# Kernel tuning notes

Hardware: AMD Instinct MI355X
Metric: run time of the kernel (lower is better)

The kernel has to match this reference:

```python
import jax, jax.numpy as jnp
import numpy as np

N, E, D, H, C, L = 10000, 160000, 512, 4, 128, 2  # nodes, edges, feat dim, heads, dim/head, layers


def setup_inputs() -> dict:
    key = jax.random.key(0)
    ks = jax.random.split(key, 16)
    s = 0.05  # weight scale (xavier-like)
    return {
        "x": jax.random.normal(ks[0], (N, D), jnp.float32),
        "edge_index": jax.random.randint(ks[1], (2, E), 0, N, dtype=jnp.int64),
        "edge_attr": jax.random.uniform(ks[2], (E, 1), jnp.float32),
        "Wq": jax.random.normal(ks[3], (L, D, H * C), jnp.float32) * s,
        "bq": jnp.zeros((L, H * C), jnp.float32),
        "Wk": jax.random.normal(ks[4], (L, D, H * C), jnp.float32) * s,
        "bk": jnp.zeros((L, H * C), jnp.float32),
        "Wv": jax.random.normal(ks[5], (L, D, H * C), jnp.float32) * s,
        "bv": jnp.zeros((L, H * C), jnp.float32),
        "We": jax.random.normal(ks[6], (L, 1, H * C), jnp.float32) * s,
        "Ws": jax.random.normal(ks[7], (L, D, H * C), jnp.float32) * s,
        "bs": jnp.zeros((L, H * C), jnp.float32),
        "gn_w": jnp.ones((L, H * C), jnp.float32),
        "gn_b": jnp.zeros((L, H * C), jnp.float32),
        "gn_ms": jnp.ones((L, H * C), jnp.float32),
    }


def _forward(x, edge_index, edge_attr, Wq, bq, Wk, bk, Wv, bv, We, Ws, bs, gn_w, gn_b, gn_ms):
    src, dst = edge_index[0], edge_index[1]
    h = x
    scale = 1.0 / jnp.sqrt(jnp.float32(C))
    for l in range(L):
        q = (h @ Wq[l] + bq[l]).reshape(N, H, C)
        k = (h @ Wk[l] + bk[l]).reshape(N, H, C)
        v = (h @ Wv[l] + bv[l]).reshape(N, H, C)
        e = (edge_attr @ We[l]).reshape(E, H, C)
        kj = k[src] + e                                    # [E,H,C]
        logits = jnp.einsum('ehc,ehc->eh', q[dst], kj) * scale  # [E,H]
        m = jax.ops.segment_max(logits, dst, num_segments=N)
        m = jnp.where(jnp.isfinite(m), m, 0.0)
        a = jnp.exp(logits - m[dst])
        denom = jax.ops.segment_sum(a, dst, num_segments=N)
        alpha = a / (denom[dst] + 1e-16)                   # scatter-softmax over in-edges
        msg = (v[src] + e) * alpha[:, :, None]             # [E,H,C]
        out = jax.ops.segment_sum(msg, dst, num_segments=N).reshape(N, H * C)
        out = out + h @ Ws[l] + bs[l]                      # root/skip connection
        # GraphNorm (single graph): mean over nodes
        mean = out.mean(0)
        sub = out - gn_ms[l] * mean
        var = (sub * sub).mean(0)
        out = gn_w[l] * sub * jax.lax.rsqrt(var + 1e-5) + gn_b[l]
        h = jax.nn.relu(out)
    xt = h.T @ h                                           # [D,D] gram matrix
    xt = (xt - xt.min()) / (xt.max() - xt.min() + 1e-8)
    iu = jnp.triu_indices(xt.shape[0], k=1)
    return xt[iu].reshape(-1, 1)


def reference(x, edge_index, edge_attr, Wq, bq, Wk, bk, Wv, bv, We, Ws, bs, gn_w, gn_b, gn_ms):
    return _forward(x, edge_index, edge_attr, Wq, bq, Wk, bk, Wv, bv, We, Ws, bs, gn_w, gn_b, gn_ms)
```

## Files before the change

### kernel.cpp

```cpp
#include <hip/hip_runtime.h>
#include <math.h>
#include <stdint.h>

typedef unsigned short u16;
typedef __attribute__((ext_vector_type(8))) _Float16 f16x8;
typedef __attribute__((ext_vector_type(4))) float f32x4;

constexpr int NN = 10000;
constexpr int NE = 160000;
constexpr int DD = 512;
constexpr int NL = 2;
constexpr int MPAD = 10112;
constexpr int K2 = 512;
constexpr int NC = 2048;
constexpr int GZ = 32;
constexpr int NKT = K2 / 32;
constexpr float SCALE = 0.08838834764831845f;

constexpr size_t B_C   = 0;
constexpr size_t B_XT  = (size_t)10016 * NC * 4;
constexpr size_t B_SM  = B_XT + (size_t)262144 * 4;
constexpr size_t B_A2  = B_SM + 32768;
constexpr size_t B_B2T = B_A2 + (size_t)MPAD * K2 * 2;
constexpr size_t B_INT = B_B2T + (size_t)2 * NC * K2 * 2;
constexpr size_t SM_CS = 0, SM_CQ = 512, SM_CA = 1024, SM_CB = 1536;
constexpr size_t SM_PMN = 2048, SM_PMX = 2304, SM_MM = 2560, SM_BIAS = 2688;
constexpr size_t I_INDPTR = 0;
constexpr size_t I_CNT    = 10016;
constexpr size_t I_CUR    = 20032;
constexpr size_t I_SSRC   = 30048;
constexpr size_t I_SATTR  = 190048;

__device__ __forceinline__ u16 f2h(float v) {
    _Float16 h = (_Float16)v;
    union { _Float16 h; u16 u; } x; x.h = h;
    return x.u;
}
__device__ __forceinline__ float h2f(u16 b) {
    union { u16 u; _Float16 h; } y; y.u = b;
    return (float)y.h;
}
__device__ __forceinline__ void gload16(const u16* g, u16* l) {
    __builtin_amdgcn_global_load_lds(
        (const __attribute__((address_space(1))) void*)g,
        (__attribute__((address_space(3))) void*)l, 16, 0, 0);
}
__device__ __forceinline__ void tile_pair(int p, int& ti, int& tj) {
    ti = (p < 4) ? 0 : (p < 7) ? 1 : (p < 9) ? 2 : 3;
    tj = p - ((ti == 0) ? 0 : (ti == 1) ? 3 : (ti == 2) ? 5 : 6);
}

__global__ void hist_kernel(const int* __restrict__ dst, int* __restrict__ cnt) {
    int e = blockIdx.x * 256 + threadIdx.x;
    if (e < NE) atomicAdd(&cnt[dst[e]], 1);
}

__global__ void scan_kernel(const int* __restrict__ cnt, int* __restrict__ indptr,
                            int* __restrict__ cur) {
    __shared__ int sh[1024];
    int tid = threadIdx.x;
    int carry = 0;
    for (int base = 0; base < NN; base += 1024) {
        int idx = base + tid;
        int v = (idx < NN) ? cnt[idx] : 0;
        sh[tid] = v;
        __syncthreads();
        #pragma unroll
        for (int off = 1; off < 1024; off <<= 1) {
            int t = (tid >= off) ? sh[tid - off] : 0;
            __syncthreads();
            sh[tid] += t;
            __syncthreads();
        }
        int incl = sh[tid];
        int excl = incl - v;
        if (idx < NN) { indptr[idx] = carry + excl; cur[idx] = carry + excl; }
        int total = sh[1023];
        __syncthreads();
        carry += total;
    }
    if (tid == 0) indptr[NN] = carry;
}

__global__ void scatter_kernel(const int* __restrict__ src, const int* __restrict__ dst,
                               const float* __restrict__ eattr, int* __restrict__ cur,
                               int* __restrict__ ssrc, float* __restrict__ sattr) {
    int e = blockIdx.x * 256 + threadIdx.x;
    if (e < NE) {
        int d = dst[e];
        int p = atomicAdd(&cur[d], 1);
        ssrc[p]  = src[e];
        sattr[p] = eattr[e];
    }
}

__global__ void convert_x_kernel(const float* __restrict__ x, u16* __restrict__ A2) {
    size_t idx = (size_t)blockIdx.x * 256 + threadIdx.x;
    if (idx >= (size_t)MPAD * 512) return;
    int r = (int)(idx >> 9), c = (int)(idx & 511);
    float v = (r < NN) ? x[(size_t)r * 512 + c] : 0.f;
    A2[(size_t)r * K2 + c] = f2h(v);
}

__global__ void convert_w_kernel(const float* __restrict__ Wq, const float* __restrict__ Wk,
                                 const float* __restrict__ Wv, const float* __restrict__ Ws,
                                 u16* __restrict__ B2T) {
    __shared__ float t[64][65];
    int bz = blockIdx.z; int l = bz >> 2, m = bz & 3;
    const float* W = (m == 0 ? Wq : m == 1 ? Wk : m == 2 ? Wv : Ws) + (size_t)l * 512 * 512;
    int k0 = blockIdx.x * 64, n0 = blockIdx.y * 64;
    int tx = threadIdx.x, ty = threadIdx.y;
    #pragma unroll
    for (int i = 0; i < 16; i++) {
        int kk = ty + 4 * i;
        t[kk][tx] = W[(size_t)(k0 + kk) * 512 + n0 + tx];
    }
    __syncthreads();
    u16* B = B2T + (size_t)l * NC * K2;
    #pragma unroll
    for (int i = 0; i < 16; i++) {
        int nn = ty + 4 * i;
        B[(size_t)(m * 512 + n0 + nn) * K2 + k0 + tx] = f2h(t[tx][nn]);
    }
}

__global__ void convert_b_kernel(const float* __restrict__ bq, const float* __restrict__ bk,
                                 const float* __restrict__ bv, const float* __restrict__ bs,
                                 float* __restrict__ biascat) {
    int idx = blockIdx.x * 256 + threadIdx.x;
    if (idx >= 2 * NC) return;
    int l = idx >> 11, c = idx & 2047;
    int m = c >> 9, j = c & 511;
    const float* b = (m == 0 ? bq : m == 1 ? bk : m == 2 ? bv : bs);
    biascat[idx] = b[l * 512 + j];
}

__global__ __launch_bounds__(256) void gemm_mfma(
    const u16* __restrict__ A2, const u16* __restrict__ B2T,
    const float* __restrict__ biasc, float* __restrict__ C)
{
    __shared__ u16 As[4096];
    __shared__ u16 Bs[4096];
    int tid = threadIdx.x;
    int wave = tid >> 6, lane = tid & 63;
    int wr = wave >> 1, wc = wave & 1;

    int bid = blockIdx.x;
    int xcd = bid & 7, qq = bid >> 3;
    int half = (qq >= 79) ? 1 : 0;
    int mb = qq - half * 79;
    int nb = xcd * 2 + half;
    int row0 = mb * 128, col0 = nb * 128;
    int mtype = nb >> 2;

    int ar0 = tid >> 2;
    int ac0 = (tid & 3) * 8;
    const u16* gA = A2  + (size_t)(row0 + ar0) * K2 + ac0;
    const u16* gB = B2T + (size_t)(col0 + ar0) * K2 + ac0;
    u16* lA = &As[wave * 512];
    u16* lB = &Bs[wave * 512];

    f32x4 acc[4][4];
    #pragma unroll
    for (int m = 0; m < 4; ++m)
        #pragma unroll
        for (int n = 0; n < 4; ++n) acc[m][n] = (f32x4){0.f, 0.f, 0.f, 0.f};

    int frow = lane & 15, fk = (lane >> 4) * 8;

    for (int kt = 0; kt < NKT; ++kt) {
        gload16(gA,             lA);
        gload16(gA + 64 * K2,   lA + 2048);
        gload16(gB,             lB);
        gload16(gB + 64 * K2,   lB + 2048);
        gA += 32; gB += 32;
        __syncthreads();
        f16x8 af[4], bfr[4];
        #pragma unroll
        for (int m = 0; m < 4; ++m)
            af[m] = *reinterpret_cast<const f16x8*>(&As[(wr * 64 + m * 16 + frow) * 32 + fk]);
        #pragma unroll
        for (int n = 0; n < 4; ++n)
            bfr[n] = *reinterpret_cast<const f16x8*>(&Bs[(wc * 64 + n * 16 + frow) * 32 + fk]);
        #pragma unroll
        for (int m = 0; m < 4; ++m)
            #pragma unroll
            for (int n = 0; n < 4; ++n)
                acc[m][n] = __builtin_amdgcn_mfma_f32_16x16x32_f16(af[m], bfr[n], acc[m][n], 0, 0, 0);
        __syncthreads();
    }

    u16* KV = (u16*)C;
    int rq = lane >> 4;
    #pragma unroll
    for (int n = 0; n < 4; ++n) {
        int gc = col0 + wc * 64 + n * 16 + frow;
        float bv = biasc[gc];
        #pragma unroll
        for (int m = 0; m < 4; ++m) {
            int gr0 = row0 + wr * 64 + m * 16 + rq * 4;
            #pragma unroll
            for (int r = 0; r < 4; ++r) {
                int gr = gr0 + r;
                if (gr < NN) {
                    float val = acc[m][n][r] + bv;
                    if (mtype == 0 || mtype == 3) C[(size_t)gr * NC + gc] = val;
                    else                          KV[(size_t)gr * 4096 + 512 + gc] = f2h(val);
                }
            }
        }
    }
}

__global__ __launch_bounds__(256) void agg_kernel(
    float* __restrict__ C, const float* __restrict__ Wel,
    const int* __restrict__ indptr, const int* __restrict__ ssrc,
    const float* __restrict__ sattr)
{
    int wid  = threadIdx.x >> 6;
    int lane = threadIdx.x & 63;
    int n = blockIdx.x * 4 + wid;
    if (n >= NN) return;
    int base = lane * 8;
    const u16* KV = (const u16*)C;

    const float4* qp = (const float4*)(C + (size_t)n * NC + base);
    float4 q0 = qp[0], q1 = qp[1];
    float qv[8] = {q0.x,q0.y,q0.z,q0.w,q1.x,q1.y,q1.z,q1.w};
    float we[8];
    #pragma unroll
    for (int j = 0; j < 8; j++) we[j] = Wel[base + j];

    float t = 0.f;
    #pragma unroll
    for (int j = 0; j < 8; j++) t = fmaf(qv[j], we[j], t);
    #pragma unroll
    for (int m = 1; m < 16; m <<= 1) t += __shfl_xor(t, m, 64);
    float qWe = t;

    float mrun = -1e30f, msum = 0.f, cattr = 0.f;
    float acc[8] = {0.f,0.f,0.f,0.f,0.f,0.f,0.f,0.f};
    int p0 = indptr[n], p1 = indptr[n + 1];
    for (int p = p0; p < p1; ++p) {
        int s = ssrc[p];
        float at = sattr[p];
        union { uint4 u; u16 h[8]; } kr, vr;
        kr.u = *(const uint4*)(KV + (size_t)s * 4096 + 1024 + base);
        float d = 0.f;
        #pragma unroll
        for (int j = 0; j < 8; j++) d = fmaf(qv[j], h2f(kr.h[j]), d);
        #pragma unroll
        for (int m = 1; m < 16; m <<= 1) d += __shfl_xor(d, m, 64);
        float logit = (d + at * qWe) * SCALE;
        float mnew = fmaxf(mrun, logit);
        float r = __expf(mrun - mnew);
        float a = __expf(logit - mnew);
        vr.u = *(const uint4*)(KV + (size_t)s * 4096 + 1536 + base);
        msum  = msum  * r + a;
        cattr = cattr * r + a * at;
        #pragma unroll
        for (int j = 0; j < 8; j++) acc[j] = acc[j] * r + a * h2f(vr.h[j]);
        mrun = mnew;
    }
    float inv = 1.f / (msum + 1e-16f);
    float* op = C + (size_t)n * NC + 1536 + base;
    float4 o0 = *(float4*)op, o1 = *(float4*)(op + 4);
    float ov[8] = {o0.x,o0.y,o0.z,o0.w,o1.x,o1.y,o1.z,o1.w};
    #pragma unroll
    for (int j = 0; j < 8; j++) ov[j] += (acc[j] + cattr * we[j]) * inv;
    *(float4*)op       = make_float4(ov[0], ov[1], ov[2], ov[3]);
    *(float4*)(op + 4) = make_float4(ov[4], ov[5], ov[6], ov[7]);
}

__global__ void colstat_kernel(const float* __restrict__ C,
                               float* __restrict__ cs, float* __restrict__ cq) {
    int c = threadIdx.x;
    int r0 = blockIdx.x * 125;
    float s0 = 0, s1 = 0, q0 = 0, q1 = 0;
    for (int r = r0; r < r0 + 125; ++r) {
        float v0 = C[(size_t)r * NC + 1536 + c];
        float v1 = C[(size_t)r * NC + 1536 + c + 256];
        s0 += v0; q0 += v0 * v0;
        s1 += v1; q1 += v1 * v1;
    }
    atomicAdd(&cs[c], s0);       atomicAdd(&cq[c], q0);
    atomicAdd(&cs[c + 256], s1); atomicAdd(&cq[c + 256], q1);
}

__global__ void coef_kernel(const float* __restrict__ cs, const float* __restrict__ cq,
                            const float* __restrict__ gnw, const float* __restrict__ gnb,
                            const float* __restrict__ gnm,
                            float* __restrict__ Aa, float* __restrict__ Bb) {
    int c = blockIdx.x * 256 + threadIdx.x;
    if (c >= DD) return;
    float mean = cs[c] * (1.f / NN);
    float ex2  = cq[c] * (1.f / NN);
    float ms = gnm[c];
    float var = ex2 - (2.f * ms - ms * ms) * mean * mean;
    float A = gnw[c] * rsqrtf(var + 1e-5f);
    Aa[c] = A;
    Bb[c] = gnb[c] - A * ms * mean;
}

__global__ void normrelu_kernel(const float* __restrict__ C, const float* __restrict__ Aa,
                                const float* __restrict__ Bb, u16* __restrict__ A2) {
    for (size_t idx = (size_t)blockIdx.x * 256 + threadIdx.x; idx < (size_t)NN * 512;
         idx += (size_t)2048 * 256) {
        int r = (int)(idx >> 9), c = (int)(idx & 511);
        float v = fmaxf(fmaf(Aa[c], C[(size_t)r * NC + 1536 + c], Bb[c]), 0.f);
        A2[(size_t)r * K2 + c] = f2h(v);
    }
}

__global__ __launch_bounds__(256) void gram_part_kernel(const u16* __restrict__ A2,
                                                        float* __restrict__ part) {
    __shared__ u16 LA[128][40], LB[128][40];
    int b = blockIdx.x;
    int p = b >> 5, z = b & (GZ - 1);
    int ti, tj; tile_pair(p, ti, tj);
    int i0c = ti * 128, j0c = tj * 128;
    int st0 = (z * 316) / GZ, st1 = ((z + 1) * 316) / GZ;

    int t = threadIdx.x;
    int c = t & 127, nb = t >> 7;
    int wave = t >> 6, lane = t & 63;
    int wr = wave >> 1, wc = wave & 1;
    int frow = lane & 15, fk = (lane >> 4) * 8, rq = lane >> 4;

    f32x4 acc[4][4];
    #pragma unroll
    for (int m = 0; m < 4; ++m)
        #pragma unroll
        for (int n = 0; n < 4; ++n) acc[m][n] = (f32x4){0.f, 0.f, 0.f, 0.f};

    for (int st = st0; st < st1; ++st) {
        int node0 = st * 32 + nb * 16;
        uint4 bufA4[2], bufB4[2];
        u16* ba = (u16*)bufA4; u16* bb = (u16*)bufB4;
        #pragma unroll
        for (int i = 0; i < 16; i++) {
            const u16* rp = A2 + (size_t)(node0 + i) * K2;
            ba[i] = rp[i0c + c];
            bb[i] = rp[j0c + c];
        }
        __syncthreads();
        *(uint4*)&LA[c][nb * 16]     = bufA4[0];
        *(uint4*)&LA[c][nb * 16 + 8] = bufA4[1];
        *(uint4*)&LB[c][nb * 16]     = bufB4[0];
        *(uint4*)&LB[c][nb * 16 + 8] = bufB4[1];
        __syncthreads();
        f16x8 af[4], bfr[4];
        #pragma unroll
        for (int m = 0; m < 4; ++m)
            af[m] = *reinterpret_cast<const f16x8*>(&LA[wr * 64 + m * 16 + frow][fk]);
        #pragma unroll
        for (int n = 0; n < 4; ++n)
            bfr[n] = *reinterpret_cast<const f16x8*>(&LB[wc * 64 + n * 16 + frow][fk]);
        #pragma unroll
        for (int m = 0; m < 4; ++m)
            #pragma unroll
            for (int n = 0; n < 4; ++n)
                acc[m][n] = __builtin_amdgcn_mfma_f32_16x16x32_f16(af[m], bfr[n], acc[m][n], 0, 0, 0);
    }

    float* pp = part + ((size_t)b << 14);
    #pragma unroll
    for (int m = 0; m < 4; ++m) {
        int li0 = wr * 64 + m * 16 + rq * 4;
        #pragma unroll
        for (int n = 0; n < 4; ++n) {
            int lj = wc * 64 + n * 16 + frow;
            #pragma unroll
            for (int r = 0; r < 4; ++r)
                pp[(li0 + r) * 128 + lj] = acc[m][n][r];
        }
    }
}

__global__ __launch_bounds__(256) void gram_reduce_kernel(const float* __restrict__ part,
                                                          float* __restrict__ xt,
                                                          float* __restrict__ pmn,
                                                          float* __restrict__ pmx) {
    __shared__ float smn[256], smx[256];
    int tid = threadIdx.x;
    int g = blockIdx.x * 1024 + tid * 4;
    int p = g >> 14, idx = g & 16383;
    const float* bp = part + ((size_t)p * GZ << 14) + idx;
    float4 s = make_float4(0.f, 0.f, 0.f, 0.f);
    #pragma unroll
    for (int z = 0; z < GZ; ++z) {
        float4 v = *(const float4*)(bp + (size_t)z * 16384);
        s.x += v.x; s.y += v.y; s.z += v.z; s.w += v.w;
    }
    int ti, tj; tile_pair(p, ti, tj);
    int li = idx >> 7, lj = idx & 127;
    *(float4*)&xt[(size_t)(ti * 128 + li) * DD + tj * 128 + lj] = s;
    float mn = fminf(fminf(s.x, s.y), fminf(s.z, s.w));
    float mx = fmaxf(fmaxf(s.x, s.y), fmaxf(s.z, s.w));
    smn[tid] = mn; smx[tid] = mx;
    __syncthreads();
    for (int st = 128; st > 0; st >>= 1) {
        if (tid < st) {
            smn[tid] = fminf(smn[tid], smn[tid + st]);
            smx[tid] = fmaxf(smx[tid], smx[tid + st]);
        }
        __syncthreads();
    }
    if (tid == 0) { pmn[blockIdx.x] = smn[0]; pmx[blockIdx.x] = smx[0]; }
}

__global__ void minmax2_kernel(const float* __restrict__ pmn, const float* __restrict__ pmx,
                               float* __restrict__ mm) {
    __shared__ float smn[256], smx[256];
    int tid = threadIdx.x;
    smn[tid] = (tid < 160) ? pmn[tid] : 1e30f;
    smx[tid] = (tid < 160) ? pmx[tid] : -1e30f;
    __syncthreads();
    for (int s = 128; s > 0; s >>= 1) {
        if (tid < s) { smn[tid] = fminf(smn[tid], smn[tid + s]); smx[tid] = fmaxf(smx[tid], smx[tid + s]); }
        __syncthreads();
    }
    if (tid == 0) { mm[0] = smn[0]; mm[1] = smx[0]; }
}

__global__ void final_kernel(const float* __restrict__ xt, const float* __restrict__ mm,
                             float* __restrict__ outp) {
    int idx = blockIdx.x * 256 + threadIdx.x;
    if (idx >= 262144) return;
    int i = idx >> 9, j = idx & 511;
    if (j <= i) return;
    float mn = mm[0], mx = mm[1];
    float v = (xt[idx] - mn) / (mx - mn + 1e-8f);
    int p = i * 511 - (i * (i - 1)) / 2 + (j - i - 1);
    outp[p] = v;
}

extern "C" void kernel_launch(void* const* d_in, const int* in_sizes, int n_in,
                              void* d_out, int out_size, void* d_ws, size_t ws_size,
                              hipStream_t stream) {
    const float* x     = (const float*)d_in[0];
    const int*   ei    = (const int*)d_in[1];
    const float* eattr = (const float*)d_in[2];
    const float* Wq = (const float*)d_in[3];  const float* bq = (const float*)d_in[4];
    const float* Wk = (const float*)d_in[5];  const float* bk = (const float*)d_in[6];
    const float* Wv = (const float*)d_in[7];  const float* bv = (const float*)d_in[8];
    const float* We = (const float*)d_in[9];
    const float* Ws = (const float*)d_in[10]; const float* bs = (const float*)d_in[11];
    const float* gnw = (const float*)d_in[12];
    const float* gnb = (const float*)d_in[13];
    const float* gnm = (const float*)d_in[14];

    char*  wsb = (char*)d_ws;
    float* C    = (float*)(wsb + B_C);
    float* xt   = (float*)(wsb + B_XT);
    float* sm   = (float*)(wsb + B_SM);
    u16*   A2   = (u16*)(wsb + B_A2);
    u16*   B2T  = (u16*)(wsb + B_B2T);
    int*   wsI  = (int*)(wsb + B_INT);

    const int* src = ei;
    const int* dst = ei + NE;

    convert_x_kernel<<<(MPAD * 512) / 256, 256, 0, stream>>>(x, A2);
    convert_w_kernel<<<dim3(8, 8, 8), dim3(64, 4), 0, stream>>>(Wq, Wk, Wv, Ws, B2T);
    convert_b_kernel<<<16, 256, 0, stream>>>(bq, bk, bv, bs, sm + SM_BIAS);

    hipMemsetAsync(wsI + I_CNT, 0, NN * sizeof(int), stream);
    hist_kernel<<<(NE + 255) / 256, 256, 0, stream>>>(dst, wsI + I_CNT);
    scan_kernel<<<1, 1024, 0, stream>>>(wsI + I_CNT, wsI + I_INDPTR, wsI + I_CUR);
    scatter_kernel<<<(NE + 255) / 256, 256, 0, stream>>>(src, dst, eattr, wsI + I_CUR,
                                                         wsI + I_SSRC, (float*)(wsI + I_SATTR));

    for (int l = 0; l < NL; ++l) {
        gemm_mfma<<<1264, 256, 0, stream>>>(A2, B2T + (size_t)l * NC * K2,
                                            sm + SM_BIAS + (size_t)l * NC, C);

        agg_kernel<<<2500, 256, 0, stream>>>(C, We + (size_t)l * DD,
                                             wsI + I_INDPTR, wsI + I_SSRC,
                                             (const float*)(wsI + I_SATTR));

        hipMemsetAsync(sm + SM_CS, 0, 1024 * sizeof(float), stream);
        colstat_kernel<<<80, 256, 0, stream>>>(C, sm + SM_CS, sm + SM_CQ);
        coef_kernel<<<2, 256, 0, stream>>>(sm + SM_CS, sm + SM_CQ,
                                           gnw + (size_t)l * DD, gnb + (size_t)l * DD,
                                           gnm + (size_t)l * DD, sm + SM_CA, sm + SM_CB);
        normrelu_kernel<<<2048, 256, 0, stream>>>(C, sm + SM_CA, sm + SM_CB, A2);
    }

    float* part = C;
    gram_part_kernel<<<10 * GZ, 256, 0, stream>>>(A2, part);
    gram_reduce_kernel<<<160, 256, 0, stream>>>(part, xt, sm + SM_PMN, sm + SM_PMX);
    minmax2_kernel<<<1, 256, 0, stream>>>(sm + SM_PMN, sm + SM_PMX, sm + SM_MM);
    final_kernel<<<1024, 256, 0, stream>>>(xt, sm + SM_MM, (float*)d_out);
}
```

Measured before the change: 351.4 us.

## Double K tile in GEMM, store Q as fp16, prefetch neighbor K/V in aggregation

The GEMM now stages 64-wide K slices per iteration with a new per-wave load layout, halving the number of barrier-separated iterations. Q is written as fp16 into the packed KV row region alongside K and V, shrinking Q traffic for the aggregation kernel. The aggregation loop is software-pipelined with two-edge lookahead prefetching of K/V rows to hide gather latency. Risks: fp16 Q reduces logit precision, and the larger LDS and register use may lower occupancy.

```diff
diff --git a/kernel.cpp b/kernel.cpp
--- a/kernel.cpp
+++ b/kernel.cpp
@@ -14,7 +14,7 @@
 constexpr int K2 = 512;
 constexpr int NC = 2048;
 constexpr int GZ = 32;
-constexpr int NKT = K2 / 32;
+constexpr int NKT = K2 / 64;
 constexpr float SCALE = 0.08838834764831845f;
 
 constexpr size_t B_C   = 0;
@@ -139,8 +139,8 @@
     const u16* __restrict__ A2, const u16* __restrict__ B2T,
     const float* __restrict__ biasc, float* __restrict__ C)
 {
-    __shared__ u16 As[4096];
-    __shared__ u16 Bs[4096];
+    __shared__ u16 As[8192];
+    __shared__ u16 Bs[8192];
     int tid = threadIdx.x;
     int wave = tid >> 6, lane = tid & 63;
     int wr = wave >> 1, wc = wave & 1;
@@ -153,12 +153,12 @@
     int row0 = mb * 128, col0 = nb * 128;
     int mtype = nb >> 2;
 
-    int ar0 = tid >> 2;
-    int ac0 = (tid & 3) * 8;
-    const u16* gA = A2  + (size_t)(row0 + ar0) * K2 + ac0;
-    const u16* gB = B2T + (size_t)(col0 + ar0) * K2 + ac0;
-    u16* lA = &As[wave * 512];
-    u16* lB = &Bs[wave * 512];
+    int l8 = lane >> 3;
+    int kofs = (lane & 7) * 8;
+    const u16* gA = A2  + (size_t)(row0 + wave * 32 + l8) * K2 + kofs;
+    const u16* gB = B2T + (size_t)(col0 + wave * 32 + l8) * K2 + kofs;
+    u16* lA = &As[wave * 2048];
+    u16* lB = &Bs[wave * 2048];
 
     f32x4 acc[4][4];
     #pragma unroll
@@ -169,24 +169,30 @@
     int frow = lane & 15, fk = (lane >> 4) * 8;
 
     for (int kt = 0; kt < NKT; ++kt) {
-        gload16(gA,             lA);
-        gload16(gA + 64 * K2,   lA + 2048);
-        gload16(gB,             lB);
-        gload16(gB + 64 * K2,   lB + 2048);
-        gA += 32; gB += 32;
-        __syncthreads();
-        f16x8 af[4], bfr[4];
-        #pragma unroll
-        for (int m = 0; m < 4; ++m)
-            af[m] = *reinterpret_cast<const f16x8*>(&As[(wr * 64 + m * 16 + frow) * 32 + fk]);
-        #pragma unroll
-        for (int n = 0; n < 4; ++n)
-            bfr[n] = *reinterpret_cast<const f16x8*>(&Bs[(wc * 64 + n * 16 + frow) * 32 + fk]);
-        #pragma unroll
-        for (int m = 0; m < 4; ++m)
+        #pragma unroll
+        for (int j = 0; j < 4; ++j) {
+            gload16(gA + j * 8 * K2, lA + j * 512);
+            gload16(gB + j * 8 * K2, lB + j * 512);
+        }
+        gA += 64; gB += 64;
+        __syncthreads();
+        #pragma unroll
+        for (int kk = 0; kk < 2; ++kk) {
+            f16x8 af[4], bfr[4];
+            #pragma unroll
+            for (int m = 0; m < 4; ++m)
+                af[m] = *reinterpret_cast<const f16x8*>(
+                    &As[(wr * 64 + m * 16 + frow) * 64 + kk * 32 + fk]);
             #pragma unroll
             for (int n = 0; n < 4; ++n)
-                acc[m][n] = __builtin_amdgcn_mfma_f32_16x16x32_f16(af[m], bfr[n], acc[m][n], 0, 0, 0);
+                bfr[n] = *reinterpret_cast<const f16x8*>(
+                    &Bs[(wc * 64 + n * 16 + frow) * 64 + kk * 32 + fk]);
+            #pragma unroll
+            for (int m = 0; m < 4; ++m)
+                #pragma unroll
+                for (int n = 0; n < 4; ++n)
+                    acc[m][n] = __builtin_amdgcn_mfma_f32_16x16x32_f16(af[m], bfr[n], acc[m][n], 0, 0, 0);
+        }
         __syncthreads();
     }
 
@@ -204,8 +210,8 @@
                 int gr = gr0 + r;
                 if (gr < NN) {
                     float val = acc[m][n][r] + bv;
-                    if (mtype == 0 || mtype == 3) C[(size_t)gr * NC + gc] = val;
-                    else                          KV[(size_t)gr * 4096 + 512 + gc] = f2h(val);
+                    if (mtype == 3) C[(size_t)gr * NC + gc] = val;
+                    else            KV[(size_t)gr * 4096 + gc] = f2h(val);
                 }
             }
         }
@@ -224,9 +230,11 @@
     int base = lane * 8;
     const u16* KV = (const u16*)C;
 
-    const float4* qp = (const float4*)(C + (size_t)n * NC + base);
-    float4 q0 = qp[0], q1 = qp[1];
-    float qv[8] = {q0.x,q0.y,q0.z,q0.w,q1.x,q1.y,q1.z,q1.w};
+    union { uint4 u; u16 h[8]; } qr;
+    qr.u = *(const uint4*)(KV + (size_t)n * 4096 + base);
+    float qv[8];
+    #pragma unroll
+    for (int j = 0; j < 8; j++) qv[j] = h2f(qr.h[j]);
     float we[8];
     #pragma unroll
     for (int j = 0; j < 8; j++) we[j] = Wel[base + j];
@@ -241,11 +249,10 @@
     float mrun = -1e30f, msum = 0.f, cattr = 0.f;
     float acc[8] = {0.f,0.f,0.f,0.f,0.f,0.f,0.f,0.f};
     int p0 = indptr[n], p1 = indptr[n + 1];
-    for (int p = p0; p < p1; ++p) {
-        int s = ssrc[p];
-        float at = sattr[p];
+
+    auto consume = [&](uint4 ku, uint4 vu, float at) {
         union { uint4 u; u16 h[8]; } kr, vr;
-        kr.u = *(const uint4*)(KV + (size_t)s * 4096 + 1024 + base);
+        kr.u = ku; vr.u = vu;
         float d = 0.f;
         #pragma unroll
         for (int j = 0; j < 8; j++) d = fmaf(qv[j], h2f(kr.h[j]), d);
@@ -255,13 +262,44 @@
         float mnew = fmaxf(mrun, logit);
         float r = __expf(mrun - mnew);
         float a = __expf(logit - mnew);
-        vr.u = *(const uint4*)(KV + (size_t)s * 4096 + 1536 + base);
         msum  = msum  * r + a;
         cattr = cattr * r + a * at;
         #pragma unroll
         for (int j = 0; j < 8; j++) acc[j] = acc[j] * r + a * h2f(vr.h[j]);
         mrun = mnew;
-    }
+    };
+
+    uint4 ka = {0,0,0,0}, va = {0,0,0,0}, kb = {0,0,0,0}, vb = {0,0,0,0};
+    float ata = 0.f, atb = 0.f;
+    if (p0 < p1) {
+        int s = ssrc[p0]; ata = sattr[p0];
+        ka = *(const uint4*)(KV + (size_t)s * 4096 + 512 + base);
+        va = *(const uint4*)(KV + (size_t)s * 4096 + 1024 + base);
+    }
+    if (p0 + 1 < p1) {
+        int s = ssrc[p0 + 1]; atb = sattr[p0 + 1];
+        kb = *(const uint4*)(KV + (size_t)s * 4096 + 512 + base);
+        vb = *(const uint4*)(KV + (size_t)s * 4096 + 1024 + base);
+    }
+    int p = p0;
+    for (; p + 1 < p1; p += 2) {
+        uint4 kc = ka, vc = va; float atc = ata;
+        if (p + 2 < p1) {
+            int s = ssrc[p + 2]; ata = sattr[p + 2];
+            ka = *(const uint4*)(KV + (size_t)s * 4096 + 512 + base);
+            va = *(const uint4*)(KV + (size_t)s * 4096 + 1024 + base);
+        }
+        consume(kc, vc, atc);
+        kc = kb; vc = vb; atc = atb;
+        if (p + 3 < p1) {
+            int s = ssrc[p + 3]; atb = sattr[p + 3];
+            kb = *(const uint4*)(KV + (size_t)s * 4096 + 512 + base);
+            vb = *(const uint4*)(KV + (size_t)s * 4096 + 1024 + base);
+        }
+        consume(kc, vc, atc);
+    }
+    if (p < p1) consume(ka, va, ata);
+
     float inv = 1.f / (msum + 1e-16f);
     float* op = C + (size_t)n * NC + 1536 + base;
     float4 o0 = *(float4*)op, o1 = *(float4*)(op + 4);
```

Result: slower. 373.4 us (+6.3%).
